# Kernel tuning notes

Measured on AMD Instinct MI355X. Metric: run time of the kernel, lower is better.

The kernel has to match this reference:

```python
import jax, jax.numpy as jnp
import numpy as np

SR = 48000
SECONDS = 2.0
T = int(SECONDS * SR)  # 96000 samples


def _shift(x, n):
    """Delay 1-D signal x by n samples, zero-filling (n may be a traced int >= 0)."""
    t = jnp.arange(x.shape[0])
    return jnp.where(t >= n, jnp.roll(x, n), jnp.zeros((), x.dtype))


def setup_inputs() -> dict:
    key = jax.random.key(0)
    k1, k2 = jax.random.split(key)
    excitation = jax.random.normal(k1, (T,), dtype=jnp.float32)
    pluckPosition = jax.random.uniform(k2, (1,), dtype=jnp.float32, minval=0.1, maxval=0.9)
    return {
        "length": 240,  # delay-line length in samples -> f0 = SR/length = 200 Hz
        "pluckPosition": pluckPosition,
        "excitation": excitation,
        "nut_gain": jnp.asarray(-0.99, jnp.float32),    # GuitarNuts reflection
        "bridge_gain": jnp.asarray(-0.995, jnp.float32),  # GuitarBridge reflection
        "bridge_b": jnp.asarray(0.5, jnp.float32),      # bridge one-zero lowpass coeff
        "disp_a": jnp.asarray(0.3, jnp.float32),        # dispersion FIR coeff
    }


def reference(length, pluckPosition, excitation, nut_gain, bridge_gain, bridge_b, disp_a):
    L = int(length)
    pluck = pluckPosition[0]
    nUp = jnp.round(L * pluck).astype(jnp.int32)   # StringSegment(nUp)
    nDown = jnp.int32(L) - nUp                      # StringSegment(nDown)

    def bridge_lp(x):
        # one-zero lowpass at the bridge: y[t] = (1-b)*x[t] + b*x[t-1]
        return (1.0 - bridge_b) * x + bridge_b * _shift(x, 1)

    def dispersion(x):
        # two-tap FIR dispersion filter: y[t] = a*x[t] + (1-a)*x[t-1]
        return disp_a * x + (1.0 - disp_a) * _shift(x, 1)

    def vibrate(l, r):
        # right-going wave: up segment -> dispersion -> down segment
        r2 = _shift(dispersion(_shift(r, nUp)), nDown)
        # left-going wave: down segment -> dispersion -> up segment
        l2 = _shift(dispersion(_shift(l, nDown)), nUp)
        return l2, r2

    # _start: inject excitation (split between the two traveling waves at pluck point)
    left0 = _shift(0.5 * excitation, nDown)
    right0 = _shift(0.5 * excitation, nUp)

    n_iter = T // L  # len(excitation) // int(length)

    def step(carry, _):
        l, r, acc = carry
        r_new = nut_gain * l                      # _lterminate: nut reflection of left wave
        l_new = bridge_gain * bridge_lp(r)        # _rterminate: bridge reflection of right wave
        l_new, r_new = vibrate(l_new, r_new)      # _vibrate: propagate through segments
        return (l_new, r_new, acc + l_new + r_new), None

    acc0 = left0 + right0
    (_, _, acc), _ = jax.lax.scan(step, (left0, right0, acc0), None, length=n_iter)
    return acc  # sum(left_signal) + sum(right_signal), shape [T]
```

## Files before the change

### kernel.cpp

```cpp
#include <hip/hip_runtime.h>


#define TPB   256
#define SAMP  4
#define CH    (TPB*SAMP)
#define MAXT  136
#define GW    8
#define ROWW  (CH + MAXT + 16)
#define ROWF  152
#define NSLOT 11
#define ESZ   3368

struct Base {
    int L, nUp, nDown;
    float gb, gn, g;
    float c0, c1, c2, d0, d1;
    float e[4];
};

static __device__ __forceinline__ Base mkbase(const int* Lp, const float* pk,
        const float* gnp, const float* gbp, const float* bbp, const float* dap) {
    Base b;
    b.L = Lp[0];
    b.gn = gnp[0]; b.gb = gbp[0];
    const float bb = bbp[0], da = dap[0];
    b.nUp   = (int)rintf((float)b.L * pk[0]);
    b.nDown = b.L - b.nUp;
    b.c0 = da * (1.f - bb);
    b.c1 = da * bb + (1.f - da) * (1.f - bb);
    b.c2 = (1.f - da) * bb;
    b.d0 = da; b.d1 = 1.f - da;
    b.e[0] = b.c0*b.d0;
    b.e[1] = b.c0*b.d1 + b.c1*b.d0;
    b.e[2] = b.c1*b.d1 + b.c2*b.d0;
    b.e[3] = b.c2*b.d1;
    b.g = b.gb * b.gn;
    return b;
}

template<int NA>
static __device__ __forceinline__ void cstepT(float* E, int ao, int bo, int co,
                                              int nc, int tid) {
    __syncthreads();
    for (int j = tid; j < nc; j += TPB) {
        float a0 = 0.f, a1 = 0.f, a2 = 0.f, a3 = 0.f;
#pragma unroll 4
        for (int i = 0; i < NA; i += 4) {
            const float4 av = *(const float4*)&E[ao + i];
            a0 += av.x * E[bo + j - i];
            a1 += av.y * E[bo + j - i - 1];
            a2 += av.z * E[bo + j - i - 2];
            a3 += av.w * E[bo + j - i - 3];
        }
        E[co + j] = (a0 + a1) + (a2 + a3);
    }
}

__global__ __launch_bounds__(TPB, 1)
void setup_kernel(const int* Lp, const float* pk, const float* __restrict__ exc,
                  const float* gnp, const float* gbp, const float* bbp, const float* dap,
                  float* __restrict__ R0, float* __restrict__ R1,
                  float* __restrict__ FIL, int* __restrict__ META, int T) {
    const Base B = mkbase(Lp, pk, gnp, gbp, bbp, dap);
    const int tid = threadIdx.x;

    if (blockIdx.x == 0) {
        __shared__ float E[ESZ];
        __shared__ int   sLo[NSLOT], sN[NSLOT];
        __shared__ float sGain[NSLOT];

        for (int i = tid; i < ESZ; i += TPB) E[i] = 0.f;
        __syncthreads();
        if (tid < 4) E[200 + tid] = B.e[tid];

        cstepT<4>  (E,  200,  200,  404,   7, tid);
        cstepT<4>  (E,  200,  404,  612,  10, tid);
        cstepT<4>  (E,  200,  612,  824,  13, tid);
        cstepT<16> (E,  824,  824, 1040,  25, tid);
        cstepT<28> (E, 1040, 1040, 1264,  49, tid);
        cstepT<28> (E, 1040, 1264, 1516,  73, tid);
        cstepT<52> (E, 1264, 1264, 1792,  97, tid);
        cstepT<100>(E, 1792, 1792, 2092, 193, tid);
        cstepT<100>(E, 1792, 2092, 2488, 289, tid);
        cstepT<196>(E, 2092, 2092, 2980, 385, tid);
        __syncthreads();

        const int esrc[NSLOT] = {200,404,612,824, 1040,1264,1516,1792,2092,2488,2980};
        const int epow[NSLOT] = {1,2,3,4, 8,16,24,32,64,96,128};

        if (tid < NSLOT) {
            const float ssum = B.e[0] + B.e[1] + B.e[2] + B.e[3];
            const float m1 = (B.e[1] + 2.f*B.e[2] + 3.f*B.e[3]) / ssum;
            const float m2 = (B.e[1] + 4.f*B.e[2] + 9.f*B.e[3]) / ssum;
            const float var = m2 - m1 * m1;
            const int P0 = 2 * B.L;
            const int p = epow[tid];
            const int full = 3 * p;
            int lo, np;
            if (tid < 4) { lo = 0; np = full + 1; }
            else {
                const float mu = p * m1, sg = sqrtf((float)p * var);
                lo = (int)floorf(mu - 6.f * sg); if (lo < 0) lo = 0; lo &= ~3;
                int hi = (int)ceilf(mu + 6.f * sg); if (hi > full) hi = full;
                np = hi - lo + 1;
            }
            np = ((np + 2) & ~3) + 1;
            if (np > MAXT - 3) {
                np = MAXT - 3;
                lo = ((int)(p * m1) - (np >> 1)) & ~3; if (lo < 0) lo = 0;
            }
            META[tid*4 + 0] = tid * MAXT;
            META[tid*4 + 1] = p * P0 + lo;
            META[tid*4 + 2] = np;
            sLo[tid] = lo; sN[tid] = np;
            float r = 1.f, bs = B.g; int pp = p;
            while (pp) { if (pp & 1) r *= bs; bs *= bs; pp >>= 1; }
            sGain[tid] = r;
        }
        __syncthreads();
        for (int sl = 0; sl < NSLOT; ++sl) {
            const int np = sN[sl], lo = sLo[sl], src = esrc[sl], full = 3 * epow[sl];
            const float gv = sGain[sl];
            for (int j = tid; j < np; j += TPB)
                FIL[sl*MAXT + j] = (lo + j <= full) ? gv * E[src + lo + j] : 0.f;
        }
    } else {
        auto ex = [&](int i) -> float { return (i >= 0) ? exc[i] : 0.f; };
        const int t0 = (blockIdx.x - 1) * CH + tid * SAMP;
#pragma unroll
        for (int u = 0; u < SAMP; ++u) {
            const int t = t0 + u;
            if (t < T) {
                const float dl = 0.5f * ex(t - B.nDown)
                    + (0.5f * B.gb) * (B.c0 * ex(t - B.L     - B.nUp)
                                     + B.c1 * ex(t - B.L - 1 - B.nUp)
                                     + B.c2 * ex(t - B.L - 2 - B.nUp));
                const float dr = 0.5f * ex(t - B.nUp)
                    + (0.5f * B.gn) * (B.d0 * ex(t - B.L     - B.nDown)
                                     + B.d1 * ex(t - B.L - 1 - B.nDown));
                R0[t] = dl; R1[t] = dr;
            }
        }
    }
}

template<int NF>
__global__ __launch_bounds__(TPB, 2)
void pass_kernel(const float* __restrict__ FIL, const int* __restrict__ META,
                 const float* __restrict__ inL, float* __restrict__ outL,
                 const float* __restrict__ inR, float* __restrict__ outR,
                 int T, int s0, int s1, int s2) {
    __shared__ float W[NF][ROWW];
    __shared__ float F[NF][ROWF];
    const int slots[3] = {s0, s1, s2};
    const float* __restrict__ X = blockIdx.y ? inR : inL;
    float* __restrict__ O       = blockIdx.y ? outR : outL;
    const int b0 = blockIdx.x * CH;
    const int tid = threadIdx.x;

    int ns[NF]; bool on[NF];
#pragma unroll
    for (int i = 0; i < NF; ++i) {
        const int off = META[slots[i]*4 + 0];
        const int dly = META[slots[i]*4 + 1];
        const int n   = META[slots[i]*4 + 2];
        ns[i] = n;
        on[i] = (b0 + CH - 1 - dly) >= 0;
        if (on[i]) {
            const int w0  = b0 - dly - n + 1;
            const int len = CH + n - 1;
            for (int idx = tid; idx < len; idx += TPB) {
                const int s = w0 + idx;
                W[i][GW + idx] = (s >= 0 && s < T) ? X[s] : 0.f;
            }
            for (int j = tid; j < ROWF; j += TPB)
                F[i][j] = (j < n) ? FIL[off + j] : 0.f;
        }
    }
    __syncthreads();

    const int t0 = b0 + tid * SAMP;
    float a0, a1, a2, a3;
    if (t0 + SAMP <= T) {
        const float4 x = *(const float4*)(X + t0);
        a0 = x.x; a1 = x.y; a2 = x.z; a3 = x.w;
    } else {
        a0 = (t0     < T) ? X[t0]     : 0.f;
        a1 = (t0 + 1 < T) ? X[t0 + 1] : 0.f;
        a2 = (t0 + 2 < T) ? X[t0 + 2] : 0.f;
        a3 = (t0 + 3 < T) ? X[t0 + 3] : 0.f;
    }

#pragma unroll
    for (int i = 0; i < NF; ++i) {
        if (!on[i]) continue;
        const int K = (ns[i] - 1) >> 2;
        const float4* W4 = (const float4*)&W[i][0];
        const float4* F4 = (const float4*)&F[i][0];
        const int Bb = (GW >> 2) + tid + K;
        float4 r1 = W4[Bb], r0 = W4[Bb - 1], rA = W4[Bb - 2];
        float4 f0 = F4[0],  fA = F4[1];
#pragma unroll 2
        for (int c = 0; c < K; ++c) {
            const float4 rN = W4[Bb - 3 - c];
            const float4 fN = F4[c + 2];
            a0 += f0.x*r1.x + f0.y*r0.w + f0.z*r0.z + f0.w*r0.y;
            a1 += f0.x*r1.y + f0.y*r1.x + f0.z*r0.w + f0.w*r0.z;
            a2 += f0.x*r1.z + f0.y*r1.y + f0.z*r1.x + f0.w*r0.w;
            a3 += f0.x*r1.w + f0.y*r1.z + f0.z*r1.y + f0.w*r1.x;
            r1 = r0; r0 = rA; rA = rN;
            f0 = fA; fA = fN;
        }
        a0 += f0.x * r1.x; a1 += f0.x * r1.y;
        a2 += f0.x * r1.z; a3 += f0.x * r1.w;
    }

    if (t0 + SAMP <= T) {
        *(float4*)(O + t0) = float4{a0, a1, a2, a3};
    } else {
        if (t0     < T) O[t0]     = a0;
        if (t0 + 1 < T) O[t0 + 1] = a1;
        if (t0 + 2 < T) O[t0 + 2] = a2;
        if (t0 + 3 < T) O[t0 + 3] = a3;
    }
}

__global__ __launch_bounds__(TPB, 2)
void pass_sum_kernel(const float* __restrict__ FIL, const int* __restrict__ META,
                     const float* __restrict__ inL, const float* __restrict__ inR,
                     float* __restrict__ out, int T, int s0) {
    __shared__ float W[ROWW];
    __shared__ float F[ROWF];
    const int b0 = blockIdx.x * CH;
    const int tid = threadIdx.x;

    const int off = META[s0*4 + 0];
    const int dly = META[s0*4 + 1];
    const int n   = META[s0*4 + 2];
    const bool on = (b0 + CH - 1 - dly) >= 0;
    if (on) {
        const int w0  = b0 - dly - n + 1;
        const int len = CH + n - 1;
        for (int idx = tid; idx < len; idx += TPB) {
            const int s = w0 + idx;
            W[GW + idx] = (s >= 0 && s < T) ? (inL[s] + inR[s]) : 0.f;
        }
        for (int j = tid; j < ROWF; j += TPB)
            F[j] = (j < n) ? FIL[off + j] : 0.f;
    }
    __syncthreads();

    const int t0 = b0 + tid * SAMP;
    float a0, a1, a2, a3;
    if (t0 + SAMP <= T) {
        const float4 xl = *(const float4*)(inL + t0);
        const float4 xr = *(const float4*)(inR + t0);
        a0 = xl.x + xr.x; a1 = xl.y + xr.y; a2 = xl.z + xr.z; a3 = xl.w + xr.w;
    } else {
        a0 = (t0     < T) ? inL[t0]     + inR[t0]     : 0.f;
        a1 = (t0 + 1 < T) ? inL[t0 + 1] + inR[t0 + 1] : 0.f;
        a2 = (t0 + 2 < T) ? inL[t0 + 2] + inR[t0 + 2] : 0.f;
        a3 = (t0 + 3 < T) ? inL[t0 + 3] + inR[t0 + 3] : 0.f;
    }

    if (on) {
        const int K = (n - 1) >> 2;
        const float4* W4 = (const float4*)&W[0];
        const float4* F4 = (const float4*)&F[0];
        const int Bb = (GW >> 2) + tid + K;
        float4 r1 = W4[Bb], r0 = W4[Bb - 1], rA = W4[Bb - 2];
        float4 f0 = F4[0],  fA = F4[1];
#pragma unroll 2
        for (int c = 0; c < K; ++c) {
            const float4 rN = W4[Bb - 3 - c];
            const float4 fN = F4[c + 2];
            a0 += f0.x*r1.x + f0.y*r0.w + f0.z*r0.z + f0.w*r0.y;
            a1 += f0.x*r1.y + f0.y*r1.x + f0.z*r0.w + f0.w*r0.z;
            a2 += f0.x*r1.z + f0.y*r1.y + f0.z*r1.x + f0.w*r0.w;
            a3 += f0.x*r1.w + f0.y*r1.z + f0.z*r1.y + f0.w*r1.x;
            r1 = r0; r0 = rA; rA = rN;
            f0 = fA; fA = fN;
        }
        a0 += f0.x * r1.x; a1 += f0.x * r1.y;
        a2 += f0.x * r1.z; a3 += f0.x * r1.w;
    }

    if (t0 + SAMP <= T) {
        *(float4*)(out + t0) = float4{a0, a1, a2, a3};
    } else {
        if (t0     < T) out[t0]     = a0;
        if (t0 + 1 < T) out[t0 + 1] = a1;
        if (t0 + 2 < T) out[t0 + 2] = a2;
        if (t0 + 3 < T) out[t0 + 3] = a3;
    }
}

extern "C" void kernel_launch(void* const* d_in, const int* in_sizes, int n_in,
                              void* d_out, int out_size, void* d_ws, size_t ws_size,
                              hipStream_t stream) {
    const int*   Lp  = (const int*)  d_in[0];
    const float* pk  = (const float*)d_in[1];
    const float* exc = (const float*)d_in[2];
    const float* gn  = (const float*)d_in[3];
    const float* gb  = (const float*)d_in[4];
    const float* bb  = (const float*)d_in[5];
    const float* da  = (const float*)d_in[6];
    float* out = (float*)d_out;
    const int T = out_size;

    float* R0   = (float*)d_ws;
    float* R1   = R0 + T;
    float* R2   = R0 + 2 * T;
    float* FIL  = R0 + 3 * T;
    int*   META = (int*)(FIL + 1536);

    const int nb = (T + CH - 1) / CH;

    setup_kernel<<<1 + nb, TPB, 0, stream>>>(Lp, pk, exc, gn, gb, bb, da,
                                             R0, R1, FIL, META, T);
    pass_kernel<3><<<dim3(nb, 2), TPB, 0, stream>>>(FIL, META, R0, R2, R1, out, T, 0, 1, 2);
    pass_kernel<1><<<dim3(nb, 2), TPB, 0, stream>>>(FIL, META, R2, R0, out, R1, T, 3, 3, 3);
    pass_kernel<3><<<dim3(nb, 2), TPB, 0, stream>>>(FIL, META, R0, R2, R1, out, T, 4, 5, 6);
    pass_kernel<3><<<dim3(nb, 2), TPB, 0, stream>>>(FIL, META, R2, R0, out, R1, T, 7, 8, 9);
    pass_sum_kernel<<<nb, TPB, 0, stream>>>(FIL, META, R0, R1, out, T, 10);
}
```

Baseline: 57.61 us.

## Merge left/right waves into one sum signal and rebalance filter-power chain

```diff
diff --git a/kernel.cpp b/kernel.cpp
--- a/kernel.cpp
+++ b/kernel.cpp
@@ -4,12 +4,12 @@
 #define TPB   256
 #define SAMP  4
 #define CH    (TPB*SAMP)
-#define MAXT  136
+#define MAXT  124
 #define GW    8
 #define ROWW  (CH + MAXT + 16)
-#define ROWF  152
-#define NSLOT 11
-#define ESZ   3368
+#define ROWF  136
+#define NSLOT 12
+#define ESZ   4176
 
 struct Base {
     int L, nUp, nDown;
@@ -59,7 +59,7 @@
 __global__ __launch_bounds__(TPB, 1)
 void setup_kernel(const int* Lp, const float* pk, const float* __restrict__ exc,
                   const float* gnp, const float* gbp, const float* bbp, const float* dap,
-                  float* __restrict__ R0, float* __restrict__ R1,
+                  float* __restrict__ Ds,
                   float* __restrict__ FIL, int* __restrict__ META, int T) {
     const Base B = mkbase(Lp, pk, gnp, gbp, bbp, dap);
     const int tid = threadIdx.x;
@@ -75,23 +75,23 @@
 
         cstepT<4>  (E,  200,  200,  404,   7, tid);
         cstepT<4>  (E,  200,  404,  612,  10, tid);
-        cstepT<4>  (E,  200,  612,  824,  13, tid);
+        cstepT<8>  (E,  404,  404,  824,  13, tid);
         cstepT<16> (E,  824,  824, 1040,  25, tid);
-        cstepT<28> (E, 1040, 1040, 1264,  49, tid);
-        cstepT<28> (E, 1040, 1264, 1516,  73, tid);
-        cstepT<52> (E, 1264, 1264, 1792,  97, tid);
-        cstepT<100>(E, 1792, 1792, 2092, 193, tid);
-        cstepT<100>(E, 1792, 2092, 2488, 289, tid);
-        cstepT<196>(E, 2092, 2092, 2980, 385, tid);
+        cstepT<16> (E,  824, 1040, 1268,  37, tid);
+        cstepT<28> (E, 1040, 1040, 1508,  49, tid);
+        cstepT<52> (E, 1508, 1508, 1760,  97, tid);
+        cstepT<52> (E, 1508, 1760, 2060, 145, tid);
+        cstepT<100>(E, 1760, 1760, 2408, 193, tid);
+        cstepT<196>(E, 2408, 2408, 2804, 385, tid);
+        cstepT<196>(E, 2408, 2804, 3392, 577, tid);
         __syncthreads();
 
-        const int esrc[NSLOT] = {200,404,612,824, 1040,1264,1516,1792,2092,2488,2980};
-        const int epow[NSLOT] = {1,2,3,4, 8,16,24,32,64,96,128};
+        const int esrc[NSLOT] = {200,404,612,824,1040,1268,1508,1760,2060,2408,2804,3392};
+        const int epow[NSLOT] = {1,2,3,4,8,12,16,32,48,64,128,192};
 
         if (tid < NSLOT) {
-            const float ssum = B.e[0] + B.e[1] + B.e[2] + B.e[3];
-            const float m1 = (B.e[1] + 2.f*B.e[2] + 3.f*B.e[3]) / ssum;
-            const float m2 = (B.e[1] + 4.f*B.e[2] + 9.f*B.e[3]) / ssum;
+            const float m1 = B.e[1] + 2.f*B.e[2] + 3.f*B.e[3];
+            const float m2 = B.e[1] + 4.f*B.e[2] + 9.f*B.e[3];
             const float var = m2 - m1 * m1;
             const int P0 = 2 * B.L;
             const int p = epow[tid];
@@ -100,8 +100,8 @@
             if (tid < 4) { lo = 0; np = full + 1; }
             else {
                 const float mu = p * m1, sg = sqrtf((float)p * var);
-                lo = (int)floorf(mu - 6.f * sg); if (lo < 0) lo = 0; lo &= ~3;
-                int hi = (int)ceilf(mu + 6.f * sg); if (hi > full) hi = full;
+                lo = (int)floorf(mu - 5.f * sg); if (lo < 0) lo = 0; lo &= ~3;
+                int hi = (int)ceilf(mu + 5.f * sg); if (hi > full) hi = full;
                 np = hi - lo + 1;
             }
             np = ((np + 2) & ~3) + 1;
@@ -138,29 +138,25 @@
                 const float dr = 0.5f * ex(t - B.nUp)
                     + (0.5f * B.gn) * (B.d0 * ex(t - B.L     - B.nDown)
                                      + B.d1 * ex(t - B.L - 1 - B.nDown));
-                R0[t] = dl; R1[t] = dr;
-            }
-        }
-    }
-}
-
-template<int NF>
+                Ds[t] = dl + dr;
+            }
+        }
+    }
+}
+
 __global__ __launch_bounds__(TPB, 2)
 void pass_kernel(const float* __restrict__ FIL, const int* __restrict__ META,
-                 const float* __restrict__ inL, float* __restrict__ outL,
-                 const float* __restrict__ inR, float* __restrict__ outR,
+                 const float* __restrict__ X, float* __restrict__ O,
                  int T, int s0, int s1, int s2) {
-    __shared__ float W[NF][ROWW];
-    __shared__ float F[NF][ROWF];
+    __shared__ float W[3][ROWW];
+    __shared__ float F[3][ROWF];
     const int slots[3] = {s0, s1, s2};
-    const float* __restrict__ X = blockIdx.y ? inR : inL;
-    float* __restrict__ O       = blockIdx.y ? outR : outL;
     const int b0 = blockIdx.x * CH;
     const int tid = threadIdx.x;
 
-    int ns[NF]; bool on[NF];
+    int ns[3]; bool on[3];
 #pragma unroll
-    for (int i = 0; i < NF; ++i) {
+    for (int i = 0; i < 3; ++i) {
         const int off = META[slots[i]*4 + 0];
         const int dly = META[slots[i]*4 + 1];
         const int n   = META[slots[i]*4 + 2];
@@ -192,7 +188,7 @@
     }
 
 #pragma unroll
-    for (int i = 0; i < NF; ++i) {
+    for (int i = 0; i < 3; ++i) {
         if (!on[i]) continue;
         const int K = (ns[i] - 1) >> 2;
         const float4* W4 = (const float4*)&W[i][0];
@@ -225,76 +221,6 @@
     }
 }
 
-__global__ __launch_bounds__(TPB, 2)
-void pass_sum_kernel(const float* __restrict__ FIL, const int* __restrict__ META,
-                     const float* __restrict__ inL, const float* __restrict__ inR,
-                     float* __restrict__ out, int T, int s0) {
-    __shared__ float W[ROWW];
-    __shared__ float F[ROWF];
-    const int b0 = blockIdx.x * CH;
-    const int tid = threadIdx.x;
-
-    const int off = META[s0*4 + 0];
-    const int dly = META[s0*4 + 1];
-    const int n   = META[s0*4 + 2];
-    const bool on = (b0 + CH - 1 - dly) >= 0;
-    if (on) {
-        const int w0  = b0 - dly - n + 1;
-        const int len = CH + n - 1;
-        for (int idx = tid; idx < len; idx += TPB) {
-            const int s = w0 + idx;
-            W[GW + idx] = (s >= 0 && s < T) ? (inL[s] + inR[s]) : 0.f;
-        }
-        for (int j = tid; j < ROWF; j += TPB)
-            F[j] = (j < n) ? FIL[off + j] : 0.f;
-    }
-    __syncthreads();
-
-    const int t0 = b0 + tid * SAMP;
-    float a0, a1, a2, a3;
-    if (t0 + SAMP <= T) {
-        const float4 xl = *(const float4*)(inL + t0);
-        const float4 xr = *(const float4*)(inR + t0);
-        a0 = xl.x + xr.x; a1 = xl.y + xr.y; a2 = xl.z + xr.z; a3 = xl.w + xr.w;
-    } else {
-        a0 = (t0     < T) ? inL[t0]     + inR[t0]     : 0.f;
-        a1 = (t0 + 1 < T) ? inL[t0 + 1] + inR[t0 + 1] : 0.f;
-        a2 = (t0 + 2 < T) ? inL[t0 + 2] + inR[t0 + 2] : 0.f;
-        a3 = (t0 + 3 < T) ? inL[t0 + 3] + inR[t0 + 3] : 0.f;
-    }
-
-    if (on) {
-        const int K = (n - 1) >> 2;
-        const float4* W4 = (const float4*)&W[0];
-        const float4* F4 = (const float4*)&F[0];
-        const int Bb = (GW >> 2) + tid + K;
-        float4 r1 = W4[Bb], r0 = W4[Bb - 1], rA = W4[Bb - 2];
-        float4 f0 = F4[0],  fA = F4[1];
-#pragma unroll 2
-        for (int c = 0; c < K; ++c) {
-            const float4 rN = W4[Bb - 3 - c];
-            const float4 fN = F4[c + 2];
-            a0 += f0.x*r1.x + f0.y*r0.w + f0.z*r0.z + f0.w*r0.y;
-            a1 += f0.x*r1.y + f0.y*r1.x + f0.z*r0.w + f0.w*r0.z;
-            a2 += f0.x*r1.z + f0.y*r1.y + f0.z*r1.x + f0.w*r0.w;
-            a3 += f0.x*r1.w + f0.y*r1.z + f0.z*r1.y + f0.w*r1.x;
-            r1 = r0; r0 = rA; rA = rN;
-            f0 = fA; fA = fN;
-        }
-        a0 += f0.x * r1.x; a1 += f0.x * r1.y;
-        a2 += f0.x * r1.z; a3 += f0.x * r1.w;
-    }
-
-    if (t0 + SAMP <= T) {
-        *(float4*)(out + t0) = float4{a0, a1, a2, a3};
-    } else {
-        if (t0     < T) out[t0]     = a0;
-        if (t0 + 1 < T) out[t0 + 1] = a1;
-        if (t0 + 2 < T) out[t0 + 2] = a2;
-        if (t0 + 3 < T) out[t0 + 3] = a3;
-    }
-}
-
 extern "C" void kernel_launch(void* const* d_in, const int* in_sizes, int n_in,
                               void* d_out, int out_size, void* d_ws, size_t ws_size,
                               hipStream_t stream) {
@@ -310,17 +236,15 @@
 
     float* R0   = (float*)d_ws;
     float* R1   = R0 + T;
-    float* R2   = R0 + 2 * T;
-    float* FIL  = R0 + 3 * T;
+    float* FIL  = R0 + 2 * T;
     int*   META = (int*)(FIL + 1536);
 
     const int nb = (T + CH - 1) / CH;
 
     setup_kernel<<<1 + nb, TPB, 0, stream>>>(Lp, pk, exc, gn, gb, bb, da,
-                                             R0, R1, FIL, META, T);
-    pass_kernel<3><<<dim3(nb, 2), TPB, 0, stream>>>(FIL, META, R0, R2, R1, out, T, 0, 1, 2);
-    pass_kernel<1><<<dim3(nb, 2), TPB, 0, stream>>>(FIL, META, R2, R0, out, R1, T, 3, 3, 3);
-    pass_kernel<3><<<dim3(nb, 2), TPB, 0, stream>>>(FIL, META, R0, R2, R1, out, T, 4, 5, 6);
-    pass_kernel<3><<<dim3(nb, 2), TPB, 0, stream>>>(FIL, META, R2, R0, out, R1, T, 7, 8, 9);
-    pass_sum_kernel<<<nb, TPB, 0, stream>>>(FIL, META, R0, R1, out, T, 10);
-}
+                                             R0, FIL, META, T);
+    pass_kernel<<<nb, TPB, 0, stream>>>(FIL, META, R0, R1, T, 0, 1, 2);
+    pass_kernel<<<nb, TPB, 0, stream>>>(FIL, META, R1, R0, T, 3, 4, 5);
+    pass_kernel<<<nb, TPB, 0, stream>>>(FIL, META, R0, R1, T, 6, 7, 8);
+    pass_kernel<<<nb, TPB, 0, stream>>>(FIL, META, R1, out, T, 9, 10, 11);
+}
```

After: 60.04 us. 1.04x slower.
